# Kernel optimization log

Hardware: AMD Instinct MI355X
Metric: run time of the kernel (lower is better)

The kernel has to match this reference:

```python
import jax, jax.numpy as jnp
import numpy as np

V, E, H, Z, K = 51, 64, 256, 32, 1000  # vocab, emb, gru hidden, latent, codebook entries
B, T = 2048, 64
COMMIT_W, QUANT_W = 0.1, 0.2


def gru(x_seq, h0, w_ih, w_hh, b_ih, b_hh):
    """torch nn.GRU (1 layer, batch_first). x_seq: (B,T,D), h0: (B,H).
    Returns (outs (B,T,H), h_last (B,H))."""
    xp = jnp.einsum('btd,gd->btg', x_seq, w_ih) + b_ih  # (B,T,3H), precompute input proj

    def step(h, xp_t):
        hp = h @ w_hh.T + b_hh
        xr, xz, xn = jnp.split(xp_t, 3, axis=-1)
        hr, hz, hn = jnp.split(hp, 3, axis=-1)
        r = jax.nn.sigmoid(xr + hr)
        zg = jax.nn.sigmoid(xz + hz)
        n = jnp.tanh(xn + r * hn)
        h_new = (1.0 - zg) * n + zg * h
        return h_new, h_new

    h_last, outs = jax.lax.scan(step, h0, jnp.swapaxes(xp, 0, 1))
    return jnp.swapaxes(outs, 0, 1), h_last


def setup_inputs() -> dict:
    key = jax.random.key(0)
    ks = jax.random.split(key, 16)
    def n(k, shape, s=0.05):
        return (jax.random.normal(k, shape, dtype=jnp.float32) * s).astype(jnp.float32)
    z32 = lambda *s: jnp.zeros(s, jnp.float32)
    return {
        'x': jax.random.randint(ks[0], (B, T), 0, V, dtype=jnp.int32),
        'enc_emb': n(ks[1], (V, E)),
        'enc_wih': n(ks[2], (3 * H, E)),
        'enc_whh': n(ks[3], (3 * H, H)),
        'enc_bih': z32(3 * H), 'enc_bhh': z32(3 * H),
        'w_mu': n(ks[4], (Z, H)), 'b_mu': z32(Z),
        'w_std': n(ks[5], (Z, H)), 'b_std': z32(Z),
        'w_q': n(ks[6], (Z, H)), 'b_q': z32(Z),
        'w_up': n(ks[7], (H, 2 * Z)), 'b_up': z32(H),
        'codebook': jax.random.uniform(ks[8], (K, Z), jnp.float32, -1.0 / K, 1.0 / K),
        'dec_emb': n(ks[9], (V, E)),
        'dec_wih': n(ks[10], (3 * H, E + 2 * Z)),
        'dec_whh': n(ks[11], (3 * H, H)),
        'dec_bih': z32(3 * H), 'dec_bhh': z32(3 * H),
        'w_out': n(ks[12], (V, H)), 'b_out': z32(V),
    }


def reference(x, enc_emb, enc_wih, enc_whh, enc_bih, enc_bhh,
              w_mu, b_mu, w_std, b_std, w_q, b_q, w_up, b_up, codebook,
              dec_emb, dec_wih, dec_whh, dec_bih, dec_bhh, w_out, b_out):
    # ---- Encoder (dropout p=0.0; eval mode) ----
    emb = enc_emb[x]                                    # (B,T,E)
    h0 = jnp.zeros((x.shape[0], H), emb.dtype)
    _, h_last = gru(emb, h0, enc_wih, enc_whh, enc_bih, enc_bhh)  # (B,H)
    mu = h_last @ w_mu.T + b_mu                         # (B,Z)
    logvar = h_last @ w_std.T + b_std
    toq = h_last @ w_q.T + b_q
    KL = jnp.sum(0.5 * (mu ** 2 + jnp.exp(logvar) - logvar - 1.0))
    z = mu  # module overrides sampled z with mu

    # ---- Vector quantization (codebook nearest neighbor) ----
    d = (jnp.sum(toq ** 2, -1, keepdims=True)
         + jnp.sum(codebook ** 2, -1)
         - 2.0 * toq @ codebook.T)                      # (B,K)
    idx = jnp.argmin(d, axis=-1)                        # (B,)
    q = codebook[idx]                                   # (B,Z)
    commitment = jnp.mean((jax.lax.stop_gradient(q) - toq) ** 2, axis=-1)
    embedding = jnp.mean((q - jax.lax.stop_gradient(toq)) ** 2, axis=-1)
    Q = jnp.sum(commitment * COMMIT_W + embedding * QUANT_W)
    q_st = toq + jax.lax.stop_gradient(q - toq)         # straight-through

    # ---- Decoder ----
    zcat = jnp.concatenate([q_st, z], axis=-1)          # (B,2Z)
    hidden = zcat @ w_up.T + b_up                       # (B,H)
    src, tgt = x[:, :-1], x[:, 1:]
    z_rep = jnp.broadcast_to(zcat[:, None, :], (x.shape[0], src.shape[1], 2 * Z))
    dec_in = jnp.concatenate([z_rep, dec_emb[src]], axis=-1)  # (B,T-1,2Z+E)
    outs, _ = gru(dec_in, hidden, dec_wih, dec_whh, dec_bih, dec_bhh)  # (B,T-1,H)
    logits = outs @ w_out.T + b_out                     # (B,T-1,V)

    logp = jax.nn.log_softmax(logits, axis=-1)
    tok_lp = jnp.take_along_axis(logp, tgt[..., None], axis=-1)[..., 0]
    mask = tgt != 0  # CrossEntropyLoss ignore_index=0, reduction='sum'
    xloss = -jnp.sum(jnp.where(mask, tok_lp, 0.0))
    nonpadded = jnp.sum(mask)
    pred_tokens = jnp.argmax(logits, axis=-1)
    return xloss, nonpadded, pred_tokens, KL, Q, idx[:, None]
```

## Files before the change

kernel.cpp:

```cpp
#include <hip/hip_runtime.h>
#include <hip/hip_bf16.h>

#define B_ 2048
#define T_ 64
#define H_ 256
#define V_ 51
#define Z_ 32
#define K_ 1000
#define LOG2E 1.4426950408889634f

typedef __bf16 bf16x8 __attribute__((ext_vector_type(8)));
typedef float floatx4 __attribute__((ext_vector_type(4)));

__device__ inline unsigned short f2bf(float f){
    unsigned int u = __float_as_uint(f);
    u += 0x7fffu + ((u >> 16) & 1u);
    return (unsigned short)(u >> 16);
}
__device__ inline float sigm2(float x){
    float e; asm("v_exp_f32 %0, -%1" : "=v"(e) : "v"(x));
    return __builtin_amdgcn_rcpf(1.0f + e);
}
__device__ inline float tanh2(float y){
    float t = y * (-2.0f*LOG2E);
    float e; asm("v_exp_f32 %0, %1" : "=v"(e) : "v"(t));
    return __builtin_fmaf(2.0f, __builtin_amdgcn_rcpf(1.0f + e), -1.0f);
}
__device__ inline float permlane_merge(float d, float s){
    asm("v_permlane32_swap_b32 %0, %1" : "+v"(d), "+v"(s));
    return d;
}
__device__ inline unsigned int cvtpk_bf16(float lo, float hi){
    unsigned int r;
    asm("v_cvt_pk_bf16_f32 %0, %1, %2" : "=v"(r) : "v"(lo), "v"(hi));
    return r;
}
__device__ inline float lo16(unsigned int u){ return __uint_as_float(u << 16); }
__device__ inline float hi16(unsigned int u){ return __uint_as_float(u & 0xffff0000u); }

#define TBLE  78336
#define PACKE 471552
#define OUTE  487936
#define PROJE 512512
#define MIDE  578048
#define CNE   579048

__device__ inline float dot64_f4(const float4* a, const float4* b){
    float s = 0.f;
    #pragma unroll
    for (int i=0;i<16;++i){
        float4 x = a[i], y = b[i];
        s = __builtin_fmaf(x.x,y.x,s); s = __builtin_fmaf(x.y,y.y,s);
        s = __builtin_fmaf(x.z,y.z,s); s = __builtin_fmaf(x.w,y.w,s);
    }
    return s;
}

__global__ __launch_bounds__(256) void k_prep(
    const float* __restrict__ enc_emb, const float* __restrict__ enc_wih, const float* __restrict__ enc_bih,
    const float* __restrict__ enc_bhh,
    const float* __restrict__ dec_emb, const float* __restrict__ dec_wih, const float* __restrict__ dec_bih,
    const float* __restrict__ dec_bhh,
    const float* __restrict__ whh_e, const float* __restrict__ whh_d, const float* __restrict__ w_out,
    const float* __restrict__ w_mu, const float* __restrict__ w_std, const float* __restrict__ w_q,
    const float* __restrict__ w_up, const float* __restrict__ cb,
    unsigned short* __restrict__ tep, unsigned short* __restrict__ tdp,
    unsigned short* __restrict__ bpe, unsigned short* __restrict__ bpd,
    unsigned short* __restrict__ bpo,
    float* __restrict__ wTproj, float* __restrict__ wTmid, float* __restrict__ cnorm)
{
    int id = blockIdx.x*256 + threadIdx.x;
    if (id < TBLE){
        int which = id / (V_*768), r = id % (V_*768);
        int v = r / 768, g = r % 768;
        int gate = g >> 8, col = g & 255;
        float s;
        if (!which){
            s = enc_bih[g] + (gate < 2 ? enc_bhh[g] : 0.0f);
            s += dot64_f4((const float4*)(enc_emb + v*64), (const float4*)(enc_wih + g*64));
            if (gate < 2) s *= LOG2E;
            tep[(v*256+col)*4 + gate] = f2bf(s);
        } else {
            s = dec_bih[g] + (gate < 2 ? dec_bhh[g] : 0.0f);
            s += dot64_f4((const float4*)(dec_emb + v*64), (const float4*)(dec_wih + g*128 + 64));
            if (gate < 2) s *= LOG2E;
            tdp[(v*256+col)*4 + gate] = f2bf(s);
        }
    } else if (id < PACKE){
        int rid = id - TBLE;
        int which = rid / 196608, e = rid % 196608;
        int j = e & 7, lane = (e>>3)&63, kt = (e>>9)&7, nt = e>>12;
        int k = kt*32 + (lane>>4)*8 + j, n = nt*16 + (lane&15);
        const float* wmat = which ? whh_d : whh_e;
        float wv = wmat[n*256+k];
        if (nt < 32) wv *= LOG2E;
        (which ? bpd : bpe)[e] = f2bf(wv);
    } else if (id < OUTE){
        int cid = id - PACKE;
        int j = cid & 7, lane = (cid>>3)&63, kt = (cid>>9)&7, nt = cid>>12;
        int k = kt*32 + (lane>>4)*8 + j, n = nt*16 + (lane&15);
        bpo[cid] = f2bf(n < V_ ? w_out[n*256+k] : 0.0f);
    } else if (id < PROJE){
        int e = id - OUTE;
        int k = e / 96, o = e % 96;
        float v = (o < 32) ? w_mu[o*H_+k] : (o < 64 ? w_std[(o-32)*H_+k] : w_q[(o-64)*H_+k]);
        wTproj[e] = v;
    } else if (id < MIDE){
        int e = id - PROJE;
        int k = e >> 10, o = e & 1023;
        float v;
        if (o < 256) v = w_up[o*64+k];
        else {
            int g = o - 256;
            v = dec_wih[(size_t)g*128 + k];
            if (g < 512) v *= LOG2E;
        }
        wTmid[e] = v;
    } else if (id < CNE){
        int k = id - MIDE;
        float s = 0.f;
        const float* cv = cb + (size_t)k*Z_;
        for (int ci=0;ci<Z_;++ci) s = __builtin_fmaf(cv[ci],cv[ci],s);
        cnorm[k] = s;
    }
}

template<int DEC>
__global__ __launch_bounds__(512, 2) void k_gru(
    const int* __restrict__ x, const unsigned short* __restrict__ tblg,
    const unsigned short* __restrict__ bpack, const float* __restrict__ bhh,
    const float* __restrict__ h0, const unsigned short* __restrict__ zvp,
    float* __restrict__ h_last, unsigned short* __restrict__ outs)
{
    const int Tn = DEC ? (T_-1) : T_;
    __shared__ alignas(16) unsigned short tbl[V_*1024];
    __shared__ alignas(16) unsigned short hbuf[2*4096];
    __shared__ unsigned int tpk[T_][2];

    const int tid = threadIdx.x;
    const int w = tid>>6, lane = tid&63, lr = lane&15, lp = lane>>4;
    const int b0 = blockIdx.x*8;
    const int jm = w + ((lane>=32)?8:0);
    const int col_m = jm*16 + lr;
    const int rbase = (lp&1)*4;
    const int colm4 = col_m*4;

    const bf16x8* bp = (const bf16x8*)bpack;
    bf16x8 wf[2][3][8];
    #pragma unroll
    for (int ji=0; ji<2; ++ji)
      #pragma unroll
      for (int g=0; g<3; ++g)
        #pragma unroll
        for (int kt=0; kt<8; ++kt)
            wf[ji][g][kt] = bp[(((g*16) + w + 8*ji)*8 + kt)*64 + lane];

    {
        uint4* d4 = (uint4*)tbl; const uint4* s4 = (const uint4*)tblg;
        for (int i=tid; i<(V_*1024)/8; i+=512) d4[i] = s4[i];
    }
    for (int i=tid; i<4096; i+=512){
        int bufi = i>>11, rr = 8 + ((i>>8)&7), c = i&255;
        hbuf[bufi*4096 + rr*256 + c] = 0;
    }
    if (tid < 128){
        int t = tid>>1, g = tid&1;
        unsigned int p = 0;
        #pragma unroll
        for (int r=0;r<4;++r) p |= ((unsigned int)x[(size_t)(b0 + g*4 + r)*T_ + t]) << (8*r);
        tpk[t][g] = p;
    }

    const float bhn = bhh[2*H_ + col_m];
    float hreg[4];
    int waddr[4];
    #pragma unroll
    for (int q=0; q<4; ++q){
        int row = rbase + q;
        float hv = DEC ? h0[(size_t)(b0+row)*H_ + col_m] : 0.0f;
        hreg[q] = hv;
        waddr[q] = row*256 + (col_m ^ (row<<3));
        hbuf[waddr[q]] = f2bf(hv);
    }
    float zr_[4], zz_[4], zn_[4];
    if (DEC){
        #pragma unroll
        for (int q=0; q<4; ++q){
            const unsigned short* zp = zvp + (((size_t)(b0+rbase+q))*256 + col_m)*4;
            uint2 zv = *(const uint2*)zp;
            zr_[q] = lo16(zv.x); zz_[q] = hi16(zv.x); zn_[q] = lo16(zv.y);
        }
    }
    const int s3 = (lr&7)<<3, lpb = lp*8;
    const int aidx0 = lr*256 + (lpb ^ s3);
    const int aidx1 = lr*256 + ((32 + lpb) ^ s3);
    const int crow = w, cc4 = lane<<2;
    const int csrc = crow*256 + (cc4 ^ (crow<<3));
    unsigned short* cdst0 = DEC ? (outs + ((size_t)(b0+crow)*(T_-1))*H_ + cc4) : nullptr;
    __syncthreads();

#define LDH(i) (*(const bf16x8*)&hbuf[(cur<<12) + (i)])
#define MFMA_(ji,g,kt,av) acc[ji][g] = __builtin_amdgcn_mfma_f32_16x16x32_bf16(av, wf[ji][g][kt], acc[ji][g], 0,0,0)

    auto step = [&](int t, int cur) {
        const int nxt = cur^1;
        unsigned int tp = tpk[t][lp&1];
        floatx4 acc[2][3] = {};

        bf16x8 a[8];
        #pragma unroll
        for (int kt=0; kt<8; ++kt)
            a[kt] = LDH(((kt&1)?aidx1:aidx0) + ((kt>>1)<<6));

        uint2 tv[4];
        #pragma unroll
        for (int q=0;q<4;++q){
            int tok = (tp >> (8*q)) & 255;
            tv[q] = *(const uint2*)&tbl[(tok<<10) + colm4];
        }

        #pragma unroll
        for (int kt=0; kt<8; ++kt){
            MFMA_(0,0,kt,a[kt]); MFMA_(1,0,kt,a[kt]);
            MFMA_(0,1,kt,a[kt]); MFMA_(1,1,kt,a[kt]);
            MFMA_(0,2,kt,a[kt]); MFMA_(1,2,kt,a[kt]);
        }

        float rg[4], zg[4], hv[4];
        #pragma unroll
        for (int q=0;q<4;++q){
            float rm = permlane_merge(acc[0][0][q], acc[1][0][q]);
            float xr = lo16(tv[q].x); if (DEC) xr += zr_[q];
            rg[q] = sigm2(xr + rm);
        }
        #pragma unroll
        for (int q=0;q<4;++q){
            float zm = permlane_merge(acc[0][1][q], acc[1][1][q]);
            float xz = hi16(tv[q].x); if (DEC) xz += zz_[q];
            zg[q] = sigm2(xz + zm);
        }
        #pragma unroll
        for (int q=0;q<4;++q){
            float nm = permlane_merge(acc[0][2][q], acc[1][2][q]);
            float xn = lo16(tv[q].y); if (DEC) xn += zn_[q];
            float ng = tanh2(__builtin_fmaf(rg[q], nm + bhn, xn));
            hv[q] = __builtin_fmaf(zg[q], hreg[q] - ng, ng);
            hreg[q] = hv[q];
        }
        unsigned int p01 = cvtpk_bf16(hv[0], hv[1]);
        unsigned int p23 = cvtpk_bf16(hv[2], hv[3]);
        hbuf[(nxt<<12) + waddr[0]] = (unsigned short)p01;
        hbuf[(nxt<<12) + waddr[1]] = (unsigned short)(p01 >> 16);
        hbuf[(nxt<<12) + waddr[2]] = (unsigned short)p23;
        hbuf[(nxt<<12) + waddr[3]] = (unsigned short)(p23 >> 16);
        __syncthreads();
        if (DEC){
            uint2 v = *(const uint2*)&hbuf[(nxt<<12) + csrc];
            *(uint2*)(cdst0 + (size_t)t*H_) = v;
        }
    };

    for (int t=0; t+1<Tn; t+=2){ step(t,0); step(t+1,1); }
    if (Tn & 1) step(Tn-1, 0);

#undef LDH
#undef MFMA_

    if (!DEC){
        #pragma unroll
        for (int q=0; q<4; ++q)
            h_last[(size_t)(b0+rbase+q)*H_ + col_m] = hreg[q];
    }
}

__global__ __launch_bounds__(256) void k_latmid(
    const float* __restrict__ hlast,
    const float* __restrict__ b_mu, const float* __restrict__ b_std, const float* __restrict__ b_q,
    const float* __restrict__ cb, const float* __restrict__ cnorm,
    const float* __restrict__ wTproj, const float* __restrict__ wTmid,
    const float* __restrict__ b_up,
    float* __restrict__ hidden, unsigned short* __restrict__ zvp,
    float* __restrict__ pKL, float* __restrict__ pQ, float* __restrict__ out_idx)
{
    __shared__ float hs[H_];
    __shared__ float pp[2][96];
    __shared__ float pout[96];
    __shared__ float zsl[64];
    __shared__ float rbuf[8];
    __shared__ int   ribuf[8];
    __shared__ int   kbc;
    const int tid = threadIdx.x;
    const int b = blockIdx.x;

    hs[tid] = hlast[(size_t)b*H_ + tid];
    __syncthreads();

    if (tid < 192){
        int o = tid % 96, kh = tid / 96;
        const float* wp = wTproj + kh*128*96 + o;
        const float* hp = hs + kh*128;
        float s = 0.f;
        #pragma unroll 8
        for (int k=0;k<128;++k) s = __builtin_fmaf(hp[k], wp[k*96], s);
        pp[kh][o] = s;
    }
    __syncthreads();
    if (tid < 96){
        float bias = (tid<32) ? b_mu[tid] : (tid<64 ? b_std[tid-32] : b_q[tid-64]);
        pout[tid] = pp[0][tid] + pp[1][tid] + bias;
    }
    __syncthreads();

    if (tid < 32){
        float m = pout[tid], l = pout[32+tid];
        float kl = 0.5f*(m*m + __expf(l) - l - 1.0f);
        #pragma unroll
        for (int off=16; off>0; off>>=1) kl += __shfl_down(kl, off, 32);
        if (tid==0) pKL[b] = kl;
    }

    const float* tq = pout + 64;
    float bd = 3.4e38f; int bk = K_;
    #pragma unroll
    for (int c4 = 0; c4 < 4; ++c4){
        int k = tid + c4*256;
        if (k < K_){
            const float4* cr = (const float4*)(cb + (size_t)k*Z_);
            float dot = 0.f;
            #pragma unroll
            for (int j=0;j<8;++j){
                float4 cv = cr[j];
                dot = __builtin_fmaf(cv.x, tq[j*4+0], dot);
                dot = __builtin_fmaf(cv.y, tq[j*4+1], dot);
                dot = __builtin_fmaf(cv.z, tq[j*4+2], dot);
                dot = __builtin_fmaf(cv.w, tq[j*4+3], dot);
            }
            float d = cnorm[k] - 2.0f*dot;
            if (d < bd){ bd = d; bk = k; }
        }
    }
    #pragma unroll
    for (int off=32; off>0; off>>=1){
        float od = __shfl_down(bd, off, 64);
        int   ok = __shfl_down(bk, off, 64);
        if (od < bd || (od == bd && ok < bk)){ bd = od; bk = ok; }
    }
    if ((tid&63)==0){ rbuf[tid>>6] = bd; ribuf[tid>>6] = bk; }
    __syncthreads();
    if (tid==0){
        float fb = rbuf[0]; int fk = ribuf[0];
        for (int wv=1; wv<4; ++wv)
            if (rbuf[wv] < fb || (rbuf[wv]==fb && ribuf[wv]<fk)){ fb=rbuf[wv]; fk=ribuf[wv]; }
        kbc = fk;
        out_idx[b] = (float)fk;
        float s = 0.f;
        const float* cv = cb + (size_t)fk*Z_;
        for (int ci=0;ci<Z_;++ci){ float df = cv[ci]-tq[ci]; s = __builtin_fmaf(df,df,s); }
        pQ[b] = s*(0.3f/32.0f);
    }
    __syncthreads();
    const int ksel = kbc;
    if (tid < 64) zsl[tid] = (tid < Z_) ? cb[(size_t)ksel*Z_ + tid] : pout[tid-Z_];
    __syncthreads();

    float a0=0.f, a1=0.f, a2=0.f, a3=0.f;
    const float* wm = wTmid + tid;
    #pragma unroll 8
    for (int k=0;k<64;++k){
        float zk = zsl[k];
        const float* wr = wm + k*1024;
        a0 = __builtin_fmaf(zk, wr[0],   a0);
        a1 = __builtin_fmaf(zk, wr[256], a1);
        a2 = __builtin_fmaf(zk, wr[512], a2);
        a3 = __builtin_fmaf(zk, wr[768], a3);
    }
    hidden[(size_t)b*H_ + tid] = a0 + b_up[tid];
    unsigned int lo = ((unsigned int)f2bf(a2) << 16) | (unsigned int)f2bf(a1);
    unsigned int hi = (unsigned int)f2bf(a3);
    *(uint2*)(zvp + ((size_t)b*256 + tid)*4) = make_uint2(lo, hi);
}

__global__ __launch_bounds__(256) void k_loss(
    const unsigned short* __restrict__ outs, const unsigned short* __restrict__ bpo,
    const float* __restrict__ b_out, const int* __restrict__ x,
    float* __restrict__ pred, float* __restrict__ pXL, float* __restrict__ pNP)
{
    __shared__ float ll[16][64];
    __shared__ float bo[64];
    __shared__ float redf[256], redn[256];
    const int tid = threadIdx.x, w = tid>>6, lane = tid&63, lr = lane&15, lp = lane>>4;
    const bf16x8* bpofr = (const bf16x8*)bpo;
    bf16x8 bw[8];
    #pragma unroll
    for (int kt=0;kt<8;++kt) bw[kt] = bpofr[(w*8+kt)*64 + lane];
    if (tid < 64) bo[tid] = (tid < V_) ? b_out[tid] : 0.0f;
    float xl = 0.f, npn = 0.f;
    const int row = tid>>4, vl = tid&15;
    for (int cc=0; cc<4; ++cc){
        int row0 = (blockIdx.x*4 + cc)*16;
        floatx4 acc = {0,0,0,0};
        #pragma unroll
        for (int kt=0;kt<8;++kt){
            bf16x8 av = *(const bf16x8*)&outs[(size_t)(row0+lr)*H_ + kt*32 + lp*8];
            acc = __builtin_amdgcn_mfma_f32_16x16x32_bf16(av, bw[kt], acc, 0,0,0);
        }
        __syncthreads();
        #pragma unroll
        for (int q=0;q<4;++q) ll[lp*4+q][w*16+lr] = acc[q];
        __syncthreads();
        float lv[4];
        #pragma unroll
        for (int k2=0;k2<4;++k2){
            int v = vl + 16*k2;
            lv[k2] = (v < V_) ? ll[row][v] + bo[v] : -3.4e38f;
        }
        float m = lv[0]; int am = vl;
        #pragma unroll
        for (int k2=1;k2<4;++k2){ if (lv[k2] > m){ m = lv[k2]; am = vl + 16*k2; } }
        #pragma unroll
        for (int off=1; off<16; off<<=1){
            float om = __shfl_xor(m, off, 16);
            int oa = __shfl_xor(am, off, 16);
            if (om > m || (om == m && oa < am)){ m = om; am = oa; }
        }
        float se = 0.f;
        #pragma unroll
        for (int k2=0;k2<4;++k2) se += __expf(lv[k2]-m);
        #pragma unroll
        for (int off=1; off<16; off<<=1) se += __shfl_xor(se, off, 16);
        if (vl == 0){
            int rowg = row0 + row;
            int b = rowg/63, tt = rowg - b*63;
            int tgt = x[(size_t)b*T_ + tt + 1];
            pred[rowg] = (float)am;
            if (tgt != 0){
                float lse = m + __logf(se);
                xl += ll[row][tgt] + bo[tgt] - lse;
                npn += 1.f;
            }
        }
    }
    redf[tid]=xl; redn[tid]=npn;
    __syncthreads();
    for (int s=128;s>0;s>>=1){ if (tid<s){ redf[tid]+=redf[tid+s]; redn[tid]+=redn[tid+s]; } __syncthreads(); }
    if (tid==0){ pXL[blockIdx.x]=redf[0]; pNP[blockIdx.x]=redn[0]; }
}

__global__ __launch_bounds__(256) void k_reduce(
    const float* __restrict__ pKL, const float* __restrict__ pQ,
    const float* __restrict__ pXL, const float* __restrict__ pNP, float* __restrict__ dout)
{
    __shared__ float r[256];
    const int tid = threadIdx.x;
    float a = 0.f;
    for (int i=tid;i<2048;i+=256) a += pKL[i];
    r[tid] = a; __syncthreads();
    for (int s=128;s>0;s>>=1){ if (tid<s) r[tid]+=r[tid+s]; __syncthreads(); }
    if (tid==0) dout[129026] = r[0];
    __syncthreads();
    a = 0.f;
    for (int i=tid;i<2048;i+=256) a += pQ[i];
    r[tid] = a; __syncthreads();
    for (int s=128;s>0;s>>=1){ if (tid<s) r[tid]+=r[tid+s]; __syncthreads(); }
    if (tid==0) dout[129027] = r[0];
    __syncthreads();
    a = 0.f;
    for (int i=tid;i<2016;i+=256) a += pXL[i];
    r[tid] = a; __syncthreads();
    for (int s=128;s>0;s>>=1){ if (tid<s) r[tid]+=r[tid+s]; __syncthreads(); }
    if (tid==0) dout[0] = -r[0];
    __syncthreads();
    a = 0.f;
    for (int i=tid;i<2016;i+=256) a += pNP[i];
    r[tid] = a; __syncthreads();
    for (int s=128;s>0;s>>=1){ if (tid<s) r[tid]+=r[tid+s]; __syncthreads(); }
    if (tid==0) dout[1] = r[0];
}

extern "C" void kernel_launch(void* const* d_in, const int* in_sizes, int n_in,
                              void* d_out, int out_size, void* d_ws, size_t ws_size,
                              hipStream_t stream)
{
    const int*   x       = (const int*)  d_in[0];
    const float* enc_emb = (const float*)d_in[1];
    const float* enc_wih = (const float*)d_in[2];
    const float* enc_whh = (const float*)d_in[3];
    const float* enc_bih = (const float*)d_in[4];
    const float* enc_bhh = (const float*)d_in[5];
    const float* w_mu    = (const float*)d_in[6];
    const float* b_mu    = (const float*)d_in[7];
    const float* w_std   = (const float*)d_in[8];
    const float* b_std   = (const float*)d_in[9];
    const float* w_q     = (const float*)d_in[10];
    const float* b_q     = (const float*)d_in[11];
    const float* w_up    = (const float*)d_in[12];
    const float* b_up    = (const float*)d_in[13];
    const float* cb      = (const float*)d_in[14];
    const float* dec_emb = (const float*)d_in[15];
    const float* dec_wih = (const float*)d_in[16];
    const float* dec_whh = (const float*)d_in[17];
    const float* dec_bih = (const float*)d_in[18];
    const float* dec_bhh = (const float*)d_in[19];
    const float* w_out   = (const float*)d_in[20];
    const float* b_out   = (const float*)d_in[21];

    float* ws = (float*)d_ws;
    unsigned short* tep = (unsigned short*)(ws + 0);
    unsigned short* tdp = (unsigned short*)(ws + 26112);
    unsigned short* bpe = (unsigned short*)(ws + 52224);
    unsigned short* bpd = (unsigned short*)(ws + 150528);
    unsigned short* bpo = (unsigned short*)(ws + 248832);
    float* hl   = ws + 257024;
    float* wTproj = ws + 781312;
    float* wTmid  = ws + 805888;
    float* cnorm  = ws + 871424;
    float* hid  = ws + 912384;
    unsigned short* zvp  = (unsigned short*)(ws + 1436672);
    unsigned short* outs = (unsigned short*)(ws + 2485248);
    float* pKL  = ws + 19000320;
    float* pQ   = ws + 19002368;
    float* pXL  = ws + 19004416;
    float* pNP  = ws + 19006432;

    float* dout = (float*)d_out;

    k_prep<<<2262,256,0,stream>>>(enc_emb, enc_wih, enc_bih, enc_bhh,
                                  dec_emb, dec_wih, dec_bih, dec_bhh,
                                  enc_whh, dec_whh, w_out,
                                  w_mu, w_std, w_q, w_up, cb,
                                  tep, tdp, bpe, bpd, bpo,
                                  wTproj, wTmid, cnorm);
    k_gru<0><<<256,512,0,stream>>>(x, tep, bpe, enc_bhh, nullptr, nullptr, hl, nullptr);
    k_latmid<<<2048,256,0,stream>>>(hl, b_mu, b_std, b_q, cb, cnorm, wTproj, wTmid, b_up,
                                    hid, zvp, pKL, pQ, dout + 129028);
    k_gru<1><<<256,512,0,stream>>>(x, tdp, bpd, dec_bhh, hid, zvp, nullptr, outs);
    k_loss<<<2016,256,0,stream>>>(outs, bpo, b_out, x, dout + 2, pXL, pNP);
    k_reduce<<<1,256,0,stream>>>(pKL, pQ, pXL, pNP, dout);
}
```

Measured before the change: 284.3 us.

## Process eight batch rows per block in latent/VQ kernel to reuse weights and codebook

The latent/quantization kernel now handles 8 batch rows per block (256 blocks instead of 2048), so each weight and codebook load from global memory is reused across 8 rows held in registers. The argmin reduction becomes a per-row shared-memory plus shuffle reduction, and the KL/Q partials are pre-summed per block, which lets the final reduce kernel read just 256 partials. The cost is more registers and shared memory per block and fewer blocks, which lowers parallelism for this kernel.

```diff
diff --git a/kernel.cpp b/kernel.cpp
--- a/kernel.cpp
+++ b/kernel.cpp
@@ -282,102 +282,139 @@
     float* __restrict__ hidden, unsigned short* __restrict__ zvp,
     float* __restrict__ pKL, float* __restrict__ pQ, float* __restrict__ out_idx)
 {
-    __shared__ float hs[H_];
-    __shared__ float pp[2][96];
-    __shared__ float pout[96];
-    __shared__ float zsl[64];
-    __shared__ float rbuf[8];
-    __shared__ int   ribuf[8];
-    __shared__ int   kbc;
+    __shared__ float hs[8][H_];
+    __shared__ float pp[2][8][96];
+    __shared__ float pout[8][96];
+    __shared__ float zsl[8][64];
+    __shared__ float dval[8][256];
+    __shared__ int   didx[8][256];
+    __shared__ float redk[8], redq[8];
+    __shared__ int   ksel[8];
     const int tid = threadIdx.x;
-    const int b = blockIdx.x;
-
-    hs[tid] = hlast[(size_t)b*H_ + tid];
+    const int b0 = blockIdx.x*8;
+
+    for (int i=tid; i<8*H_; i+=256) hs[i>>8][i&255] = hlast[(size_t)b0*H_ + i];
     __syncthreads();
 
     if (tid < 192){
         int o = tid % 96, kh = tid / 96;
         const float* wp = wTproj + kh*128*96 + o;
-        const float* hp = hs + kh*128;
-        float s = 0.f;
-        #pragma unroll 8
-        for (int k=0;k<128;++k) s = __builtin_fmaf(hp[k], wp[k*96], s);
-        pp[kh][o] = s;
-    }
-    __syncthreads();
-    if (tid < 96){
-        float bias = (tid<32) ? b_mu[tid] : (tid<64 ? b_std[tid-32] : b_q[tid-64]);
-        pout[tid] = pp[0][tid] + pp[1][tid] + bias;
-    }
-    __syncthreads();
-
-    if (tid < 32){
-        float m = pout[tid], l = pout[32+tid];
+        float s[8] = {0,0,0,0,0,0,0,0};
+        for (int k=0;k<128;++k){
+            float wv = wp[k*96];
+            #pragma unroll
+            for (int r=0;r<8;++r) s[r] = __builtin_fmaf(hs[r][kh*128+k], wv, s[r]);
+        }
+        #pragma unroll
+        for (int r=0;r<8;++r) pp[kh][r][o] = s[r];
+    }
+    __syncthreads();
+    for (int id=tid; id<768; id+=256){
+        int o = id % 96, r = id / 96;
+        float bias = (o<32) ? b_mu[o] : (o<64 ? b_std[o-32] : b_q[o-64]);
+        pout[r][o] = pp[0][r][o] + pp[1][r][o] + bias;
+    }
+    __syncthreads();
+
+    {
+        int r = tid>>5, zi = tid&31;
+        float m = pout[r][zi], l = pout[r][32+zi];
         float kl = 0.5f*(m*m + __expf(l) - l - 1.0f);
         #pragma unroll
         for (int off=16; off>0; off>>=1) kl += __shfl_down(kl, off, 32);
-        if (tid==0) pKL[b] = kl;
-    }
-
-    const float* tq = pout + 64;
-    float bd = 3.4e38f; int bk = K_;
-    #pragma unroll
-    for (int c4 = 0; c4 < 4; ++c4){
+        if (zi==0) redk[r] = kl;
+    }
+
+    float best[8]; int bi[8];
+    #pragma unroll
+    for (int r=0;r<8;++r){ best[r] = 3.4e38f; bi[r] = K_; }
+    #pragma unroll
+    for (int c4=0; c4<4; ++c4){
         int k = tid + c4*256;
         if (k < K_){
             const float4* cr = (const float4*)(cb + (size_t)k*Z_);
-            float dot = 0.f;
+            float4 cv[8];
             #pragma unroll
-            for (int j=0;j<8;++j){
-                float4 cv = cr[j];
-                dot = __builtin_fmaf(cv.x, tq[j*4+0], dot);
-                dot = __builtin_fmaf(cv.y, tq[j*4+1], dot);
-                dot = __builtin_fmaf(cv.z, tq[j*4+2], dot);
-                dot = __builtin_fmaf(cv.w, tq[j*4+3], dot);
+            for (int j=0;j<8;++j) cv[j] = cr[j];
+            float cn = cnorm[k];
+            #pragma unroll
+            for (int r=0;r<8;++r){
+                float dot = 0.f;
+                #pragma unroll
+                for (int j=0;j<8;++j){
+                    dot = __builtin_fmaf(cv[j].x, pout[r][64+j*4+0], dot);
+                    dot = __builtin_fmaf(cv[j].y, pout[r][64+j*4+1], dot);
+                    dot = __builtin_fmaf(cv[j].z, pout[r][64+j*4+2], dot);
+                    dot = __builtin_fmaf(cv[j].w, pout[r][64+j*4+3], dot);
+                }
+                float d = __builtin_fmaf(-2.0f, dot, cn);
+                if (d < best[r]){ best[r] = d; bi[r] = k; }
             }
-            float d = cnorm[k] - 2.0f*dot;
-            if (d < bd){ bd = d; bk = k; }
-        }
-    }
-    #pragma unroll
-    for (int off=32; off>0; off>>=1){
-        float od = __shfl_down(bd, off, 64);
-        int   ok = __shfl_down(bk, off, 64);
-        if (od < bd || (od == bd && ok < bk)){ bd = od; bk = ok; }
-    }
-    if ((tid&63)==0){ rbuf[tid>>6] = bd; ribuf[tid>>6] = bk; }
+        }
+    }
+    #pragma unroll
+    for (int r=0;r<8;++r){ dval[r][tid] = best[r]; didx[r][tid] = bi[r]; }
+    __syncthreads();
+    {
+        int r = tid>>5, c = tid&31;
+        float bm = 3.4e38f; int bx = K_+1;
+        #pragma unroll
+        for (int e=0;e<8;++e){
+            int j = c + e*32;
+            float dv = dval[r][j]; int di = didx[r][j];
+            if (dv < bm || (dv == bm && di < bx)){ bm = dv; bx = di; }
+        }
+        #pragma unroll
+        for (int off=16; off>0; off>>=1){
+            float om = __shfl_xor(bm, off, 32);
+            int   oi = __shfl_xor(bx, off, 32);
+            if (om < bm || (om == bm && oi < bx)){ bm = om; bx = oi; }
+        }
+        if (c == 0){
+            ksel[r] = bx;
+            out_idx[b0+r] = (float)bx;
+            float s = 0.f;
+            const float* cv = cb + (size_t)bx*Z_;
+            for (int ci=0;ci<Z_;++ci){ float df = cv[ci]-pout[r][64+ci]; s = __builtin_fmaf(df,df,s); }
+            redq[r] = s*(0.3f/32.0f);
+        }
+    }
     __syncthreads();
     if (tid==0){
-        float fb = rbuf[0]; int fk = ribuf[0];
-        for (int wv=1; wv<4; ++wv)
-            if (rbuf[wv] < fb || (rbuf[wv]==fb && ribuf[wv]<fk)){ fb=rbuf[wv]; fk=ribuf[wv]; }
-        kbc = fk;
-        out_idx[b] = (float)fk;
-        float s = 0.f;
-        const float* cv = cb + (size_t)fk*Z_;
-        for (int ci=0;ci<Z_;++ci){ float df = cv[ci]-tq[ci]; s = __builtin_fmaf(df,df,s); }
-        pQ[b] = s*(0.3f/32.0f);
-    }
-    __syncthreads();
-    const int ksel = kbc;
-    if (tid < 64) zsl[tid] = (tid < Z_) ? cb[(size_t)ksel*Z_ + tid] : pout[tid-Z_];
-    __syncthreads();
-
-    float a0=0.f, a1=0.f, a2=0.f, a3=0.f;
+        float q=0.f, kl=0.f;
+        #pragma unroll
+        for (int r=0;r<8;++r){ q += redq[r]; kl += redk[r]; }
+        pQ[blockIdx.x] = q; pKL[blockIdx.x] = kl;
+    }
+    for (int id=tid; id<512; id+=256){
+        int r = id>>6, cc = id&63;
+        zsl[r][cc] = (cc < Z_) ? cb[(size_t)ksel[r]*Z_ + cc] : pout[r][cc-Z_];
+    }
+    __syncthreads();
+
+    float a0[8]={0,0,0,0,0,0,0,0}, a1[8]={0,0,0,0,0,0,0,0};
+    float a2[8]={0,0,0,0,0,0,0,0}, a3[8]={0,0,0,0,0,0,0,0};
     const float* wm = wTmid + tid;
-    #pragma unroll 8
     for (int k=0;k<64;++k){
-        float zk = zsl[k];
         const float* wr = wm + k*1024;
-        a0 = __builtin_fmaf(zk, wr[0],   a0);
-        a1 = __builtin_fmaf(zk, wr[256], a1);
-        a2 = __builtin_fmaf(zk, wr[512], a2);
-        a3 = __builtin_fmaf(zk, wr[768], a3);
-    }
-    hidden[(size_t)b*H_ + tid] = a0 + b_up[tid];
-    unsigned int lo = ((unsigned int)f2bf(a2) << 16) | (unsigned int)f2bf(a1);
-    unsigned int hi = (unsigned int)f2bf(a3);
-    *(uint2*)(zvp + ((size_t)b*256 + tid)*4) = make_uint2(lo, hi);
+        float w0 = wr[0], w1 = wr[256], w2 = wr[512], w3 = wr[768];
+        #pragma unroll
+        for (int r=0;r<8;++r){
+            float zk = zsl[r][k];
+            a0[r] = __builtin_fmaf(zk, w0, a0[r]);
+            a1[r] = __builtin_fmaf(zk, w1, a1[r]);
+            a2[r] = __builtin_fmaf(zk, w2, a2[r]);
+            a3[r] = __builtin_fmaf(zk, w3, a3[r]);
+        }
+    }
+    float bup = b_up[tid];
+    #pragma unroll
+    for (int r=0;r<8;++r){
+        hidden[(size_t)(b0+r)*H_ + tid] = a0[r] + bup;
+        unsigned int lo = ((unsigned int)f2bf(a2[r]) << 16) | (unsigned int)f2bf(a1[r]);
+        unsigned int hi = (unsigned int)f2bf(a3[r]);
+        *(uint2*)(zvp + ((size_t)(b0+r)*256 + tid)*4) = make_uint2(lo, hi);
+    }
 }
 
 __global__ __launch_bounds__(256) void k_loss(
@@ -452,19 +489,15 @@
 {
     __shared__ float r[256];
     const int tid = threadIdx.x;
-    float a = 0.f;
-    for (int i=tid;i<2048;i+=256) a += pKL[i];
-    r[tid] = a; __syncthreads();
+    r[tid] = pKL[tid]; __syncthreads();
     for (int s=128;s>0;s>>=1){ if (tid<s) r[tid]+=r[tid+s]; __syncthreads(); }
     if (tid==0) dout[129026] = r[0];
     __syncthreads();
-    a = 0.f;
-    for (int i=tid;i<2048;i+=256) a += pQ[i];
-    r[tid] = a; __syncthreads();
+    r[tid] = pQ[tid]; __syncthreads();
     for (int s=128;s>0;s>>=1){ if (tid<s) r[tid]+=r[tid+s]; __syncthreads(); }
     if (tid==0) dout[129027] = r[0];
     __syncthreads();
-    a = 0.f;
+    float a = 0.f;
     for (int i=tid;i<2016;i+=256) a += pXL[i];
     r[tid] = a; __syncthreads();
     for (int s=128;s>0;s>>=1){ if (tid<s) r[tid]+=r[tid+s]; __syncthreads(); }
@@ -531,8 +564,8 @@
                                   tep, tdp, bpe, bpd, bpo,
                                   wTproj, wTmid, cnorm);
     k_gru<0><<<256,512,0,stream>>>(x, tep, bpe, enc_bhh, nullptr, nullptr, hl, nullptr);
-    k_latmid<<<2048,256,0,stream>>>(hl, b_mu, b_std, b_q, cb, cnorm, wTproj, wTmid, b_up,
-                                    hid, zvp, pKL, pQ, dout + 129028);
+    k_latmid<<<256,256,0,stream>>>(hl, b_mu, b_std, b_q, cb, cnorm, wTproj, wTmid, b_up,
+                                   hid, zvp, pKL, pQ, dout + 129028);
     k_gru<1><<<256,512,0,stream>>>(x, tdp, bpd, dec_bhh, hid, zvp, nullptr, outs);
     k_loss<<<2016,256,0,stream>>>(outs, bpo, b_out, x, dout + 2, pXL, pNP);
     k_reduce<<<1,256,0,stream>>>(pKL, pQ, pXL, pNP, dout);
```

Result: faster. 258.4 us (median of 2 runs) (-9.1%).
